# Kernel optimization log

Hardware: AMD Instinct MI355X
Metric: run time of the kernel (lower is better)

Reference implementation:

```python
import jax, jax.numpy as jnp
import numpy as np

S, W = 256, 64          # sentences per doc, words per sentence
V, E = 100000, 256      # vocab, embedding dim
HW, HS, C = 256, 256, 10  # word hidden, sentence hidden, num categories


def _gru_dir(x, Wih, Whh, bih, bhh, reverse):
    """Single-direction GRU, PyTorch gate order (r, z, n). x: [B, T, D] -> [B, T, H]."""
    B, T, D = x.shape
    H = Whh.shape[1]
    xg = jnp.einsum('btd,gd->tbg', x, Wih) + bih  # [T, B, 3H], precompute input gates

    def step(h, xt):
        hg = h @ Whh.T + bhh
        xr, xz, xn = jnp.split(xt, 3, axis=-1)
        hr, hz, hn = jnp.split(hg, 3, axis=-1)
        r = jax.nn.sigmoid(xr + hr)
        z = jax.nn.sigmoid(xz + hz)
        n = jnp.tanh(xn + r * hn)
        h_new = (1.0 - z) * n + z * h
        return h_new, h_new

    h0 = jnp.zeros((B, H), x.dtype)
    _, ys = jax.lax.scan(step, h0, xg, reverse=reverse)  # ys: [T, B, H] in time order
    return jnp.swapaxes(ys, 0, 1)


def _bi_gru(x, WihF, WhhF, bihF, bhhF, WihB, WhhB, bihB, bhhB):
    out_f = _gru_dir(x, WihF, WhhF, bihF, bhhF, reverse=False)
    out_b = _gru_dir(x, WihB, WhhB, bihB, bhhB, reverse=True)
    return jnp.concatenate([out_f, out_b], axis=-1)  # [B, T, 2H]


def _attn_pool(out, w, b):
    # Sequential(Linear(2H,1), Tanh) then softmax over seq dim, weighted sum
    scores = jnp.tanh(out @ w + b)           # [B, T, 1]
    a = jax.nn.softmax(scores, axis=1)       # softmax over time
    return jnp.sum(a * out, axis=1)          # [B, 2H]


def setup_inputs() -> dict:
    key = jax.random.key(0)
    ks = jax.random.split(key, 32)
    sc = 0.05
    d = {
        'tokens': jax.random.randint(ks[0], (S, W), 0, V),
        'emb': jax.random.normal(ks[1], (V, E), jnp.float32) * sc,
        'wWihF': jax.random.normal(ks[2], (3 * HW, E), jnp.float32) * sc,
        'wWhhF': jax.random.normal(ks[3], (3 * HW, HW), jnp.float32) * sc,
        'wBihF': jax.random.normal(ks[4], (3 * HW,), jnp.float32) * sc,
        'wBhhF': jax.random.normal(ks[5], (3 * HW,), jnp.float32) * sc,
        'wWihB': jax.random.normal(ks[6], (3 * HW, E), jnp.float32) * sc,
        'wWhhB': jax.random.normal(ks[7], (3 * HW, HW), jnp.float32) * sc,
        'wBihB': jax.random.normal(ks[8], (3 * HW,), jnp.float32) * sc,
        'wBhhB': jax.random.normal(ks[9], (3 * HW,), jnp.float32) * sc,
        'sWihF': jax.random.normal(ks[10], (3 * HS, 2 * HW), jnp.float32) * sc,
        'sWhhF': jax.random.normal(ks[11], (3 * HS, HS), jnp.float32) * sc,
        'sBihF': jax.random.normal(ks[12], (3 * HS,), jnp.float32) * sc,
        'sBhhF': jax.random.normal(ks[13], (3 * HS,), jnp.float32) * sc,
        'sWihB': jax.random.normal(ks[14], (3 * HS, 2 * HW), jnp.float32) * sc,
        'sWhhB': jax.random.normal(ks[15], (3 * HS, HS), jnp.float32) * sc,
        'sBihB': jax.random.normal(ks[16], (3 * HS,), jnp.float32) * sc,
        'sBhhB': jax.random.normal(ks[17], (3 * HS,), jnp.float32) * sc,
        'wAttW': jax.random.normal(ks[18], (2 * HW, 1), jnp.float32) * sc,
        'wAttB': jax.random.normal(ks[19], (1,), jnp.float32) * sc,
        'sAttW': jax.random.normal(ks[20], (2 * HS, 1), jnp.float32) * sc,
        'sAttB': jax.random.normal(ks[21], (1,), jnp.float32) * sc,
        'clsW': jax.random.normal(ks[22], (C, 2 * HS), jnp.float32) * sc,
        'clsB': jax.random.normal(ks[23], (C,), jnp.float32) * sc,
    }
    return d


def reference(tokens, emb, wWihF, wWhhF, wBihF, wBhhF, wWihB, wWhhB, wBihB, wBhhB,
              sWihF, sWhhF, sBihF, sBhhF, sWihB, sWhhB, sBihB, sBhhB,
              wAttW, wAttB, sAttW, sAttB, clsW, clsB):
    # word level: all sentences batched together (packed form of the Python loop)
    x = emb[tokens]                                             # [S, W, E]
    word_out = _bi_gru(x, wWihF, wWhhF, wBihF, wBhhF, wWihB, wWhhB, wBihB, wBhhB)  # [S, W, 2HW]
    sent_vecs = _attn_pool(word_out, wAttW, wAttB)              # [S, 2HW]
    # sentence level: single document
    sent_in = sent_vecs[None]                                   # [1, S, 2HW]
    sent_out = _bi_gru(sent_in, sWihF, sWhhF, sBihF, sBhhF, sWihB, sWhhB, sBihB, sBhhB)  # [1, S, 2HS]
    doc_vec = _attn_pool(sent_out, sAttW, sAttB)                # [1, 2HS]
    logits = doc_vec @ clsW.T + clsB                            # [1, C]
    return jax.nn.softmax(logits, axis=1)
```

## Files before the change

kernel.cpp:

```cpp
#include <hip/hip_runtime.h>
#include <stdint.h>

typedef unsigned short ushort_t;
typedef uint32_t u32;
typedef __bf16 bf16;
typedef bf16 bf16x8 __attribute__((ext_vector_type(8)));
typedef float f32x4 __attribute__((ext_vector_type(4)));
typedef ushort_t ushort8 __attribute__((ext_vector_type(8)));

__device__ __forceinline__ float b2f(ushort_t u) {
    u32 x = ((u32)u) << 16;
    return __builtin_bit_cast(float, x);
}
__device__ __forceinline__ ushort_t f2b(float f) {
    bf16 h = (bf16)f;
    return __builtin_bit_cast(ushort_t, h);
}
__device__ __forceinline__ float sigmoidf_(float x) { return 1.0f / (1.0f + __expf(-x)); }
__device__ __forceinline__ float tanhf_(float x) { return 1.0f - 2.0f / (1.0f + __expf(2.0f * x)); }

__device__ __forceinline__ ushort8 cvt8(const float* __restrict__ p) {
    float4 v0 = *(const float4*)p;
    float4 v1 = *(const float4*)(p + 4);
    ushort8 r;
    r[0] = f2b(v0.x); r[1] = f2b(v0.y); r[2] = f2b(v0.z); r[3] = f2b(v0.w);
    r[4] = f2b(v1.x); r[5] = f2b(v1.y); r[6] = f2b(v1.z); r[7] = f2b(v1.w);
    return r;
}

#define TPAD 40

__global__ __launch_bounds__(256) void gemm_xg(
    const float* __restrict__ A, const int* __restrict__ tok,
    const float* __restrict__ WF, const float* __restrict__ WB,
    const float* __restrict__ bF, const float* __restrict__ bB,
    ushort_t* __restrict__ C, int K)
{
    __shared__ ushort_t aT[128 * TPAD];
    __shared__ ushort_t bT[128 * TPAD];
    const int tid = threadIdx.x;
    const int lane = tid & 63, wv = tid >> 6;
    const int bn0 = blockIdx.x * 128;
    const int rm0 = blockIdx.y * 128;
    const int wm = (wv & 1) * 64, wn = (wv >> 1) * 64;

    f32x4 acc[4][4];
    f32x4 zero = {0.f, 0.f, 0.f, 0.f};
#pragma unroll
    for (int i = 0; i < 4; i++)
#pragma unroll
        for (int j = 0; j < 4; j++) acc[i][j] = zero;

    const int sr = tid >> 1;
    const int sk = (tid & 1) * 16;
    long arow = tok ? (long)tok[rm0 + sr] : (long)(rm0 + sr);
    const float* aSrc = A + arow * K + sk;
    int ng = bn0 + sr;
    const float* bSrc = (ng < 768 ? WF + (long)ng * K : WB + (long)(ng - 768) * K) + sk;

    const int nkc = K / 32;
    const int fm = lane & 15, fq = (lane >> 4) * 8;
    for (int kc = 0; kc < nkc; ++kc) {
        ushort8 av0 = cvt8(aSrc + kc * 32);
        ushort8 av1 = cvt8(aSrc + kc * 32 + 8);
        ushort8 bv0 = cvt8(bSrc + kc * 32);
        ushort8 bv1 = cvt8(bSrc + kc * 32 + 8);
        __syncthreads();
        *(ushort8*)(aT + sr * TPAD + sk) = av0;
        *(ushort8*)(aT + sr * TPAD + sk + 8) = av1;
        *(ushort8*)(bT + sr * TPAD + sk) = bv0;
        *(ushort8*)(bT + sr * TPAD + sk + 8) = bv1;
        __syncthreads();
        bf16x8 af[4], bfg[4];
#pragma unroll
        for (int i = 0; i < 4; i++)
            af[i] = __builtin_bit_cast(bf16x8, *(const ushort8*)(aT + (wm + i * 16 + fm) * TPAD + fq));
#pragma unroll
        for (int j = 0; j < 4; j++)
            bfg[j] = __builtin_bit_cast(bf16x8, *(const ushort8*)(bT + (wn + j * 16 + fm) * TPAD + fq));
#pragma unroll
        for (int i = 0; i < 4; i++)
#pragma unroll
            for (int j = 0; j < 4; j++)
                acc[i][j] = __builtin_amdgcn_mfma_f32_16x16x32_bf16(af[i], bfg[j], acc[i][j], 0, 0, 0);
    }
    const int fr0 = (lane >> 4) * 4;
#pragma unroll
    for (int j = 0; j < 4; j++) {
        int col = bn0 + wn + j * 16 + fm;
        float bias = (col < 768) ? bF[col] : bB[col - 768];
#pragma unroll
        for (int i = 0; i < 4; i++) {
#pragma unroll
            for (int r = 0; r < 4; r++) {
                int row = rm0 + wm + i * 16 + fr0 + r;
                C[(long)row * 1536 + col] = f2b(acc[i][j][r] + bias);
            }
        }
    }
}

#define XRS 776
#define ORS 264

template<int NS, int CS>
__global__ __launch_bounds__(512, 2) void gru_level(
    const float* __restrict__ WhhF, const float* __restrict__ WhhB,
    const float* __restrict__ bhhF, const float* __restrict__ bhhB,
    const ushort_t* __restrict__ xg,
    ushort_t* __restrict__ out,
    int T)
{
    __shared__ ushort_t afrag[2][8 * 512];
    __shared__ ushort_t xch[2][16 * XRS];
    __shared__ ushort_t och[2][16 * ORS];

    const int tid = threadIdx.x, lane = tid & 63, wv = tid >> 6;
    const int dir = blockIdx.x & 1;
    const int grp = blockIdx.x >> 1;
    const float* Whh = dir ? WhhB : WhhF;
    const float* bhh = dir ? bhhB : bhhF;
    const int dirOff = dir * 768;

    const int fm = lane & 15;
    const int mgrp = lane >> 4;
    const int d0 = 32 * wv + fm;

    bf16x8 wfrag[6][8];
#pragma unroll
    for (int g = 0; g < 3; ++g)
#pragma unroll
        for (int t = 0; t < 2; ++t) {
            const float* wrow = Whh + (long)(g * 256 + 32 * wv + 16 * t + fm) * 256 + mgrp * 8;
#pragma unroll
            for (int kc = 0; kc < 8; ++kc)
                wfrag[g * 2 + t][kc] = __builtin_bit_cast(bf16x8, cvt8(wrow + kc * 32));
        }

    float bhhv[3][2];
#pragma unroll
    for (int g = 0; g < 3; ++g)
#pragma unroll
        for (int t = 0; t < 2; ++t)
            bhhv[g][t] = bhh[g * 256 + d0 + 16 * t];

    for (int i = tid; i < 8 * 512; i += 512) { afrag[0][i] = 0; afrag[1][i] = 0; }

    const int s0 = grp * NS;
    const ushort_t* xgm0 = xg + (long)s0 * T * 1536 + dirOff;
    const ushort_t* xgm1 = xg + (long)(s0 + (NS > 1 ? 1 : 0)) * T * 1536 + dirOff;
    ushort_t* outm0 = out + (long)s0 * T * 512 + dir * 256;
    ushort_t* outm1 = out + (long)(s0 + (NS > 1 ? 1 : 0)) * T * 512 + dir * 256;

    float h[NS][2];
#pragma unroll
    for (int m = 0; m < NS; ++m) { h[m][0] = 0.f; h[m][1] = 0.f; }

    const int nch = T / CS;

    auto stage_x = [&](int c2) {
        ushort8 val[3];
        int row[3], c8[3];
#pragma unroll
        for (int i = 0; i < 3; ++i) {
            int v = tid + i * 512;
            row[i] = v / 96; c8[i] = v - row[i] * 96;
            int sc = row[i] / NS, m = row[i] - sc * NS;
            int stg = c2 * CS + sc;
            int tt = dir ? (T - 1 - stg) : stg;
            const ushort_t* xp = (NS == 1 || m == 0) ? xgm0 : xgm1;
            val[i] = *(const ushort8*)(xp + (long)tt * 1536 + c8[i] * 8);
        }
#pragma unroll
        for (int i = 0; i < 3; ++i)
            *(ushort8*)(&xch[c2 & 1][row[i] * XRS + c8[i] * 8]) = val[i];
    };

    auto flush_o = [&](int c2) {
        int v = tid;
        int row = v >> 5, c8 = v & 31;
        int sc = row / NS, m = row - sc * NS;
        int stg = c2 * CS + sc;
        int tt = dir ? (T - 1 - stg) : stg;
        ushort8 val = *(const ushort8*)(&och[c2 & 1][row * ORS + c8 * 8]);
        ushort_t* op = (NS == 1 || m == 0) ? outm0 : outm1;
        *(ushort8*)(op + (long)tt * 512 + c8 * 8) = val;
    };

    stage_x(0);
    __syncthreads();

#define LDA(BUF, KC) __builtin_bit_cast(bf16x8, *(const ushort8*)(&afrag[BUF][(KC) * 512 + lane * 8]))
#define MF6(AV, KC) { _Pragma("unroll") for (int gi = 0; gi < 6; ++gi) \
    acc[gi] = __builtin_amdgcn_mfma_f32_16x16x32_bf16(AV, wfrag[gi][KC], acc[gi], 0, 0, 0); }

    for (int c = 0; c < nch; ++c) {
        const int buf = c & 1;
        if (c > 0) flush_o(c - 1);
        if (c + 1 < nch) stage_x(c + 1);
        for (int sc = 0; sc < CS; ++sc) {
            const int st = c * CS + sc;
            const int cur = st & 1, nxt = cur ^ 1;
            ushort_t xv[NS][3][2];
            if (mgrp == 0) {
#pragma unroll
                for (int m = 0; m < NS; ++m) {
                    const int xrow = (sc * NS + m) * XRS;
#pragma unroll
                    for (int g = 0; g < 3; ++g)
#pragma unroll
                        for (int t = 0; t < 2; ++t)
                            xv[m][g][t] = xch[buf][xrow + g * 256 + d0 + 16 * t];
                }
            }
            f32x4 acc[6];
            f32x4 zero = {0.f, 0.f, 0.f, 0.f};
#pragma unroll
            for (int gi = 0; gi < 6; ++gi) acc[gi] = zero;
            {
                bf16x8 t0 = LDA(cur, 0), t1 = LDA(cur, 1), t2 = LDA(cur, 2);
                MF6(t0, 0); t0 = LDA(cur, 3);
                MF6(t1, 1); t1 = LDA(cur, 4);
                MF6(t2, 2); t2 = LDA(cur, 5);
                MF6(t0, 3); t0 = LDA(cur, 6);
                MF6(t1, 4); t1 = LDA(cur, 7);
                MF6(t2, 5);
                MF6(t0, 6);
                MF6(t1, 7);
            }
            if (mgrp == 0) {
#pragma unroll
                for (int m = 0; m < NS; ++m) {
#pragma unroll
                    for (int t = 0; t < 2; ++t) {
                        float xr = b2f(xv[m][0][t]);
                        float xz = b2f(xv[m][1][t]);
                        float xn = b2f(xv[m][2][t]);
                        float r = sigmoidf_(xr + acc[0 + t][m] + bhhv[0][t]);
                        float z = sigmoidf_(xz + acc[2 + t][m] + bhhv[1][t]);
                        float n = tanhf_(xn + r * (acc[4 + t][m] + bhhv[2][t]));
                        h[m][t] = (1.f - z) * n + z * h[m][t];
                        ushort_t hb = f2b(h[m][t]);
                        afrag[nxt][wv * 512 + ((2 * t + (fm >> 3)) * 16 + m) * 8 + (fm & 7)] = hb;
                        och[buf][(sc * NS + m) * ORS + d0 + 16 * t] = hb;
                    }
                }
            }
            __syncthreads();
        }
    }
    flush_o(nch - 1);
#undef LDA
#undef MF6
}

__global__ void attn_word(const ushort_t* __restrict__ wout,
                          const float* __restrict__ attW,
                          const float* __restrict__ attB,
                          float* __restrict__ svec)
{
    __shared__ float part[64][4];
    __shared__ float aw[64];
    const int s = blockIdx.x, tid = threadIdx.x;
    const int w = tid >> 2, q = tid & 3;
    const ushort_t* row = wout + ((long)(s * 64 + w)) * 512 + q * 128;
    const float* ap = attW + q * 128;
    float sum = 0.f;
    for (int i = 0; i < 128; i += 8) {
        ushort8 a = *(const ushort8*)(row + i);
        float4 b0 = *(const float4*)(ap + i);
        float4 b1 = *(const float4*)(ap + i + 4);
        sum += b2f(a[0]) * b0.x + b2f(a[1]) * b0.y + b2f(a[2]) * b0.z + b2f(a[3]) * b0.w
             + b2f(a[4]) * b1.x + b2f(a[5]) * b1.y + b2f(a[6]) * b1.z + b2f(a[7]) * b1.w;
    }
    part[w][q] = sum;
    __syncthreads();
    if (tid < 64) {
        float sc = tanhf_(part[tid][0] + part[tid][1] + part[tid][2] + part[tid][3] + attB[0]);
        float m = sc;
#pragma unroll
        for (int o = 32; o >= 1; o >>= 1) m = fmaxf(m, __shfl_xor(m, o, 64));
        float e = __expf(sc - m);
        float se = e;
#pragma unroll
        for (int o = 32; o >= 1; o >>= 1) se += __shfl_xor(se, o, 64);
        aw[tid] = e / se;
    }
    __syncthreads();
    const int d = tid * 2;
    float a0 = 0.f, a1 = 0.f;
    const ushort_t* col = wout + ((long)(s * 64)) * 512 + d;
#pragma unroll 4
    for (int w2 = 0; w2 < 64; ++w2) {
        u32 v = *(const u32*)(col + (long)w2 * 512);
        float wg = aw[w2];
        a0 += wg * b2f((ushort_t)v);
        a1 += wg * b2f((ushort_t)(v >> 16));
    }
    *(float2*)(svec + (long)s * 512 + d) = make_float2(a0, a1);
}

__global__ void attn_sent(const ushort_t* __restrict__ sout,
                          const float* __restrict__ attW,
                          const float* __restrict__ attB,
                          float* __restrict__ doc)
{
    __shared__ float aw[256];
    __shared__ float red[8];
    const int tid = threadIdx.x;
    const ushort_t* row = sout + (long)tid * 512;
    float sum = 0.f;
    for (int i = 0; i < 512; i += 8) {
        ushort8 a = *(const ushort8*)(row + i);
        float4 b0 = *(const float4*)(attW + i);
        float4 b1 = *(const float4*)(attW + i + 4);
        sum += b2f(a[0]) * b0.x + b2f(a[1]) * b0.y + b2f(a[2]) * b0.z + b2f(a[3]) * b0.w
             + b2f(a[4]) * b1.x + b2f(a[5]) * b1.y + b2f(a[6]) * b1.z + b2f(a[7]) * b1.w;
    }
    float sc = tanhf_(sum + attB[0]);
    float m = sc;
#pragma unroll
    for (int o = 32; o >= 1; o >>= 1) m = fmaxf(m, __shfl_xor(m, o, 64));
    if ((tid & 63) == 0) red[tid >> 6] = m;
    __syncthreads();
    m = fmaxf(fmaxf(red[0], red[1]), fmaxf(red[2], red[3]));
    float e = __expf(sc - m);
    float se = e;
#pragma unroll
    for (int o = 32; o >= 1; o >>= 1) se += __shfl_xor(se, o, 64);
    if ((tid & 63) == 0) red[4 + (tid >> 6)] = se;
    __syncthreads();
    se = red[4] + red[5] + red[6] + red[7];
    aw[tid] = e / se;
    __syncthreads();
    const int d = tid * 2;
    float a0 = 0.f, a1 = 0.f;
    for (int t2 = 0; t2 < 256; ++t2) {
        u32 v = *(const u32*)(sout + (long)t2 * 512 + d);
        float w = aw[t2];
        a0 += w * b2f((ushort_t)v);
        a1 += w * b2f((ushort_t)(v >> 16));
    }
    doc[d] = a0;
    doc[d + 1] = a1;
}

__global__ void classify(const float* __restrict__ doc, const float* __restrict__ clsW,
                         const float* __restrict__ clsB, float* __restrict__ outp)
{
    const int lane = threadIdx.x;
    float logit = -1e30f;
    if (lane < 10) {
        float s = clsB[lane];
        const float* wr = clsW + lane * 512;
        for (int i = 0; i < 512; ++i) s += doc[i] * wr[i];
        logit = s;
    }
    float m = logit;
#pragma unroll
    for (int o = 32; o >= 1; o >>= 1) m = fmaxf(m, __shfl_xor(m, o, 64));
    float e = (lane < 10) ? __expf(logit - m) : 0.f;
    float se = e;
#pragma unroll
    for (int o = 32; o >= 1; o >>= 1) se += __shfl_xor(se, o, 64);
    if (lane < 10) outp[lane] = e / se;
}

extern "C" void kernel_launch(void* const* d_in, const int* in_sizes, int n_in,
                              void* d_out, int out_size, void* d_ws, size_t ws_size,
                              hipStream_t stream)
{
    const int*   tokens = (const int*)d_in[0];
    const float* emb    = (const float*)d_in[1];
    const float* wWihF  = (const float*)d_in[2];
    const float* wWhhF  = (const float*)d_in[3];
    const float* wBihF  = (const float*)d_in[4];
    const float* wBhhF  = (const float*)d_in[5];
    const float* wWihB  = (const float*)d_in[6];
    const float* wWhhB  = (const float*)d_in[7];
    const float* wBihB  = (const float*)d_in[8];
    const float* wBhhB  = (const float*)d_in[9];
    const float* sWihF  = (const float*)d_in[10];
    const float* sWhhF  = (const float*)d_in[11];
    const float* sBihF  = (const float*)d_in[12];
    const float* sBhhF  = (const float*)d_in[13];
    const float* sWihB  = (const float*)d_in[14];
    const float* sWhhB  = (const float*)d_in[15];
    const float* sBihB  = (const float*)d_in[16];
    const float* sBhhB  = (const float*)d_in[17];
    const float* wAttW  = (const float*)d_in[18];
    const float* wAttB  = (const float*)d_in[19];
    const float* sAttW  = (const float*)d_in[20];
    const float* sAttB  = (const float*)d_in[21];
    const float* clsW   = (const float*)d_in[22];
    const float* clsB   = (const float*)d_in[23];

    char* ws = (char*)d_ws;
    ushort_t* xg   = (ushort_t*)(ws);
    ushort_t* wout = (ushort_t*)(ws + 50331648);
    float*    svec = (float*)(ws + 67108864);
    ushort_t* sxg  = (ushort_t*)(ws + 67633152);
    ushort_t* sout = (ushort_t*)(ws + 68419584);
    float*    doc  = (float*)(ws + 68681728);

    gemm_xg<<<dim3(12, 128), 256, 0, stream>>>(emb, tokens, wWihF, wWihB, wBihF, wBihB, xg, 256);
    gru_level<2, 8><<<256, 512, 0, stream>>>(wWhhF, wWhhB, wBhhF, wBhhB, xg, wout, 64);
    attn_word<<<256, 256, 0, stream>>>(wout, wAttW, wAttB, svec);
    gemm_xg<<<dim3(12, 2), 256, 0, stream>>>(svec, nullptr, sWihF, sWihB, sBihF, sBihB, sxg, 512);
    gru_level<1, 16><<<2, 512, 0, stream>>>(sWhhF, sWhhB, sBhhF, sBhhB, sxg, sout, 256);
    attn_sent<<<1, 256, 0, stream>>>(sout, sAttW, sAttB, doc);
    classify<<<1, 64, 0, stream>>>(doc, clsW, clsB, (float*)d_out);
}
```

Baseline: 823.6 us.

## Add register-resident fp16 dot2 kernel for sentence-level GRU recurrence

Replaces the generic MFMA-based GRU kernel for the sentence level (batch 1, 256 sequential steps) with a dedicated kernel of 768 threads. Each thread holds one row of Whh packed as fp16 pairs in registers and computes its gate preactivation with fdot2 against the hidden state broadcast from shared memory. The aim is to cut per-step latency on this latency-bound, batch-1 recurrence, where MFMA tiles are mostly wasted. The cost is 128 registers of weights per thread, fp16 precision for the recurrent matmul, and two barriers per step.

Measured after the change: 880.5 us. 6.9% more time.

```diff
diff --git a/kernel.cpp b/kernel.cpp
--- a/kernel.cpp
+++ b/kernel.cpp
@@ -7,6 +7,8 @@
 typedef bf16 bf16x8 __attribute__((ext_vector_type(8)));
 typedef float f32x4 __attribute__((ext_vector_type(4)));
 typedef ushort_t ushort8 __attribute__((ext_vector_type(8)));
+typedef _Float16 f16;
+typedef f16 f16x2v __attribute__((ext_vector_type(2)));
 
 __device__ __forceinline__ float b2f(ushort_t u) {
     u32 x = ((u32)u) << 16;
@@ -18,6 +20,20 @@
 }
 __device__ __forceinline__ float sigmoidf_(float x) { return 1.0f / (1.0f + __expf(-x)); }
 __device__ __forceinline__ float tanhf_(float x) { return 1.0f - 2.0f / (1.0f + __expf(2.0f * x)); }
+
+__device__ __forceinline__ u32 packf16(float a, float b) {
+    f16 ha = (f16)a, hb = (f16)b;
+    return (u32)__builtin_bit_cast(ushort_t, ha) | ((u32)__builtin_bit_cast(ushort_t, hb) << 16);
+}
+__device__ __forceinline__ float fdot2_(u32 w, u32 h, float acc) {
+#if __has_builtin(__builtin_amdgcn_fdot2)
+    return __builtin_amdgcn_fdot2(__builtin_bit_cast(f16x2v, w),
+                                  __builtin_bit_cast(f16x2v, h), acc, false);
+#else
+    f16x2v a = __builtin_bit_cast(f16x2v, w), b = __builtin_bit_cast(f16x2v, h);
+    return acc + (float)a.x * (float)b.x + (float)a.y * (float)b.y;
+#endif
+}
 
 __device__ __forceinline__ ushort8 cvt8(const float* __restrict__ p) {
     float4 v0 = *(const float4*)p;
@@ -252,6 +268,97 @@
     flush_o(nch - 1);
 #undef LDA
 #undef MF6
+}
+
+__global__ __launch_bounds__(768, 3) void gru_sent(
+    const float* __restrict__ WhhF, const float* __restrict__ WhhB,
+    const float* __restrict__ bhhF, const float* __restrict__ bhhB,
+    const ushort_t* __restrict__ xg,
+    ushort_t* __restrict__ out,
+    int T)
+{
+    __shared__ ushort_t h2ld[256];
+    __shared__ float preact[768];
+    __shared__ ushort_t xch[2][16 * XRS];
+    __shared__ ushort_t och[2][16 * ORS];
+
+    const int tid = threadIdx.x;
+    const int dir = blockIdx.x;
+    const float* Whh = dir ? WhhB : WhhF;
+    const float* bhh = dir ? bhhB : bhhF;
+    const int dirOff = dir * 768;
+
+    u32 w2r[128];
+#pragma unroll
+    for (int q = 0; q < 64; ++q) {
+        float4 v = *(const float4*)(Whh + (long)tid * 256 + q * 4);
+        w2r[2 * q]     = packf16(v.x, v.y);
+        w2r[2 * q + 1] = packf16(v.z, v.w);
+    }
+    const int d = tid;
+    float bh_r = 0.f, bh_z = 0.f, bh_n = 0.f, h = 0.f;
+    if (tid < 256) { bh_r = bhh[d]; bh_z = bhh[256 + d]; bh_n = bhh[512 + d]; }
+    for (int i = tid; i < 256; i += 768) h2ld[i] = 0;
+
+    const int nch = T / 16;
+    auto stage_x = [&](int c2) {
+#pragma unroll
+        for (int i = 0; i < 2; ++i) {
+            int v = tid + i * 768;
+            int row = v / 96, c8 = v - row * 96;
+            int stg = c2 * 16 + row;
+            int tt = dir ? (T - 1 - stg) : stg;
+            ushort8 val = *(const ushort8*)(xg + (long)tt * 1536 + dirOff + c8 * 8);
+            *(ushort8*)(&xch[c2 & 1][row * XRS + c8 * 8]) = val;
+        }
+    };
+    auto flush_o = [&](int c2) {
+        if (tid < 512) {
+            int row = tid >> 5, c8 = tid & 31;
+            int stg = c2 * 16 + row;
+            int tt = dir ? (T - 1 - stg) : stg;
+            ushort8 val = *(const ushort8*)(&och[c2 & 1][row * ORS + c8 * 8]);
+            *(ushort8*)(out + (long)tt * 512 + dir * 256 + c8 * 8) = val;
+        }
+    };
+    stage_x(0);
+    __syncthreads();
+
+    for (int c = 0; c < nch; ++c) {
+        const int buf = c & 1;
+        if (c > 0) flush_o(c - 1);
+        if (c + 1 < nch) stage_x(c + 1);
+        for (int sc = 0; sc < 16; ++sc) {
+            float xr = 0.f, xz = 0.f, xn = 0.f;
+            if (tid < 256) {
+                xr = b2f(xch[buf][sc * XRS + d]);
+                xz = b2f(xch[buf][sc * XRS + 256 + d]);
+                xn = b2f(xch[buf][sc * XRS + 512 + d]);
+            }
+            float acc = 0.f;
+#pragma unroll
+            for (int q = 0; q < 32; ++q) {
+                uint4 hv = *(const uint4*)(&h2ld[q * 8]);
+                acc = fdot2_(w2r[4 * q + 0], hv.x, acc);
+                acc = fdot2_(w2r[4 * q + 1], hv.y, acc);
+                acc = fdot2_(w2r[4 * q + 2], hv.z, acc);
+                acc = fdot2_(w2r[4 * q + 3], hv.w, acc);
+            }
+            preact[tid] = acc;
+            __syncthreads();
+            if (tid < 256) {
+                float r = sigmoidf_(xr + preact[d] + bh_r);
+                float z = sigmoidf_(xz + preact[256 + d] + bh_z);
+                float n = tanhf_(xn + r * (preact[512 + d] + bh_n));
+                h = (1.f - z) * n + z * h;
+                f16 hf = (f16)h;
+                h2ld[d] = __builtin_bit_cast(ushort_t, hf);
+                och[buf][sc * ORS + d] = f2b(h);
+            }
+            __syncthreads();
+        }
+    }
+    flush_o(nch - 1);
 }
 
 __global__ void attn_word(const ushort_t* __restrict__ wout,
@@ -407,7 +514,7 @@
     gru_level<2, 8><<<256, 512, 0, stream>>>(wWhhF, wWhhB, wBhhF, wBhhB, xg, wout, 64);
     attn_word<<<256, 256, 0, stream>>>(wout, wAttW, wAttB, svec);
     gemm_xg<<<dim3(12, 2), 256, 0, stream>>>(svec, nullptr, sWihF, sWihB, sBihF, sBihB, sxg, 512);
-    gru_level<1, 16><<<2, 512, 0, stream>>>(sWhhF, sWhhB, sBhhF, sBhhB, sxg, sout, 256);
+    gru_sent<<<2, 768, 0, stream>>>(sWhhF, sWhhB, sBhhF, sBhhB, sxg, sout, 256);
     attn_sent<<<1, 256, 0, stream>>>(sout, sAttW, sAttB, doc);
     classify<<<1, 64, 0, stream>>>(doc, clsW, clsB, (float*)d_out);
 }
```
